# Kernel optimization log

Measured on AMD Instinct MI355X. Metric: run time of the kernel, lower is better.

Reference implementation:

```python
import jax, jax.numpy as jnp
import numpy as np

B, S, D, H = 4, 2048, 1024, 16
DEPTH = D // H
NEG = -1e9


def setup_inputs() -> dict:
    key = jax.random.key(0)
    ks = jax.random.split(key, 10)
    scale = 1.0 / np.sqrt(D)
    return {
        "query": jax.random.normal(ks[0], (B, S, D), jnp.float32),
        "key": jax.random.normal(ks[1], (B, S, D), jnp.float32),
        "value": jax.random.normal(ks[2], (B, S, D), jnp.float32),
        "mask": jnp.zeros((B, 1, 1, S), jnp.float32),
        "Wq": jax.random.normal(ks[3], (D, D), jnp.float32) * scale,
        "bq": jnp.zeros((D,), jnp.float32),
        "Wk": jax.random.normal(ks[4], (D, D), jnp.float32) * scale,
        "bk": jnp.zeros((D,), jnp.float32),
        "Wv": jax.random.normal(ks[5], (D, D), jnp.float32) * scale,
        "bv": jnp.zeros((D,), jnp.float32),
        "Wo": jax.random.normal(ks[6], (D, D), jnp.float32) * scale,
        "bo": jnp.zeros((D,), jnp.float32),
    }


def _split_heads(x):
    # [B, S, D] -> [B, H, S, depth]
    b, s, _ = x.shape
    return x.reshape(b, s, H, DEPTH).transpose(0, 2, 1, 3)


def reference(query, key, value, mask, Wq, bq, Wk, bk, Wv, bv, Wo, bo):
    q = _split_heads(query @ Wq + bq)
    k = _split_heads(key @ Wk + bk)
    v = _split_heads(value @ Wv + bv)
    # scaled dot-product attention
    logits = jnp.einsum("bhqd,bhkd->bhqk", q, k) / jnp.sqrt(
        jnp.asarray(DEPTH, jnp.float32))
    logits = logits + mask * NEG
    attn = jax.nn.softmax(logits, axis=-1)
    out = jnp.einsum("bhqk,bhkd->bhqd", attn, v)
    # merge heads: [B,H,S,depth] -> [B,S,D]
    out = out.transpose(0, 2, 1, 3).reshape(query.shape[0], -1, D)
    out = out @ Wo + bo
    return out, attn
```

## Files before the change

kernel.cpp:

```cpp
#include <hip/hip_runtime.h>
#include <stdint.h>


typedef float f32x4 __attribute__((ext_vector_type(4)));
typedef __bf16 bf16x8 __attribute__((ext_vector_type(8)));
typedef unsigned short u16x4 __attribute__((ext_vector_type(4)));
typedef unsigned short u16x8 __attribute__((ext_vector_type(8)));

#define LOG2E 1.44269504088896340736f

static __device__ __forceinline__ f32x4 mfma16(bf16x8 a, bf16x8 b, f32x4 c) {
  return __builtin_amdgcn_mfma_f32_16x16x32_bf16(a, b, c, 0, 0, 0);
}
static __device__ __forceinline__ unsigned short bfc(float f) {
  return __builtin_bit_cast(unsigned short, (__bf16)f);
}
static __device__ __forceinline__ float e2(float x) { return __builtin_amdgcn_exp2f(x); }

#define GLDS16(g, l)                                                    \
  __builtin_amdgcn_global_load_lds(                                     \
      (const __attribute__((address_space(1))) void*)(g),               \
      (__attribute__((address_space(3))) void*)(l), 16, 0, 0)

struct Ptr3 { const float* s[3]; unsigned short* d[3]; };
struct Ptr4 { const float* s[4]; unsigned short* d[4]; };
struct QKArgs {
  const unsigned short* A[2];
  const unsigned short* Bt[2];
  const float* bias[2];
  unsigned short* C[2];
};

__global__ void cvt3(Ptr3 p) {
  const int z = blockIdx.z;
  const int i = (blockIdx.x * 256 + threadIdx.x) * 4;
  f32x4 v = *(const f32x4*)(const void*)(p.s[z] + i);
  u16x4 o;
  o[0] = bfc(v[0]); o[1] = bfc(v[1]); o[2] = bfc(v[2]); o[3] = bfc(v[3]);
  *(u16x4*)(void*)(p.d[z] + i) = o;
}

__global__ void wtrans4(Ptr4 p) {
  __shared__ float t[32][33];
  const int z = blockIdx.z;
  const float* W = p.s[z];
  unsigned short* Wt = p.d[z];
  const int tx = threadIdx.x & 31, ty = threadIdx.x >> 5;
  const int n0 = blockIdx.x * 32, k0 = blockIdx.y * 32;
#pragma unroll
  for (int i = 0; i < 4; ++i)
    t[ty + i * 8][tx] = W[(size_t)(k0 + ty + i * 8) * 1024 + n0 + tx];
  __syncthreads();
#pragma unroll
  for (int i = 0; i < 4; ++i)
    Wt[(size_t)(n0 + ty + i * 8) * 1024 + k0 + tx] = bfc(t[tx][ty + i * 8]);
}

#define GEMM_PROLOG(Aptr, Btptr)                                        \
  __shared__ unsigned short sA[128 * 32];                               \
  __shared__ unsigned short sB[128 * 32];                               \
  const int tid = threadIdx.x;                                          \
  const int m0 = blockIdx.x << 7, n0 = blockIdx.y << 7;                 \
  const int w = tid >> 6, lane = tid & 63, g = lane >> 4, r = lane & 15;\
  const int wr = w >> 1, wc = w & 1;                                    \
  const int srow = tid >> 2;                                            \
  const int scol = (tid & 3) << 3;                                      \
  const unsigned short* ga = (Aptr) + (size_t)(m0 + srow) * 1024 + scol;\
  const unsigned short* gb = (Btptr) + (size_t)(n0 + srow) * 1024 + scol;\
  unsigned short* la = sA + tid * 8;                                    \
  unsigned short* lb = sB + tid * 8;

#define GEMM_KLOOP(SWAP)                                                \
  for (int kt = 0; kt < 32; ++kt) {                                     \
    const int ko = kt << 5;                                             \
    GLDS16(ga + ko, la);                                                \
    GLDS16(ga + ko + 64 * 1024, la + 64 * 32);                          \
    GLDS16(gb + ko, lb);                                                \
    GLDS16(gb + ko + 64 * 1024, lb + 64 * 32);                          \
    __syncthreads();                                                    \
    bf16x8 af[4], bfv[4];                                               \
    _Pragma("unroll")                                                   \
    for (int i = 0; i < 4; ++i) {                                       \
      af[i]  = *(const bf16x8*)(const void*)&sA[(wr * 64 + i * 16 + r) * 32 + g * 8]; \
      bfv[i] = *(const bf16x8*)(const void*)&sB[(wc * 64 + i * 16 + r) * 32 + g * 8]; \
    }                                                                   \
    _Pragma("unroll")                                                   \
    for (int i = 0; i < 4; ++i)                                         \
      _Pragma("unroll")                                                 \
      for (int j = 0; j < 4; ++j)                                       \
        acc[i][j] = (SWAP) ? mfma16(bfv[j], af[i], acc[i][j])           \
                           : mfma16(af[i], bfv[j], acc[i][j]);          \
    __syncthreads();                                                    \
  }

__global__ __launch_bounds__(256, 2) void gemm_qk(QKArgs args) {
  const int z = blockIdx.z;
  const f32x4 fz = {0.f, 0.f, 0.f, 0.f};
  f32x4 acc[4][4];
#pragma unroll
  for (int i = 0; i < 4; ++i)
#pragma unroll
    for (int j = 0; j < 4; ++j) acc[i][j] = fz;
  GEMM_PROLOG(args.A[z], args.Bt[z])
  GEMM_KLOOP(1)
  const float osc = (z == 0) ? (0.125f * LOG2E) : 1.0f;
  unsigned short* Cq = args.C[z];
  const float* bias = args.bias[z];
#pragma unroll
  for (int j = 0; j < 4; ++j) {
    const int nb = n0 + wc * 64 + j * 16 + g * 4;
    const f32x4 b4 = *(const f32x4*)(const void*)(bias + nb);
#pragma unroll
    for (int i = 0; i < 4; ++i) {
      const int m = m0 + wr * 64 + i * 16 + r;
      const int bb = m >> 11, s = m & 2047, hh = nb >> 6, d = nb & 63;
      u16x4 pk;
#pragma unroll
      for (int t = 0; t < 4; ++t) pk[t] = bfc((acc[i][j][t] + b4[t]) * osc);
      *(u16x4*)(void*)(Cq + (size_t)(bb * 16 + hh) * 131072 + (size_t)s * 64 + d) = pk;
    }
  }
}

__global__ __launch_bounds__(256, 2) void gemm_v(const unsigned short* __restrict__ A,
                                                 const unsigned short* __restrict__ Bt,
                                                 const float* __restrict__ bias,
                                                 unsigned short* __restrict__ C) {
  const f32x4 fz = {0.f, 0.f, 0.f, 0.f};
  f32x4 acc[4][4];
#pragma unroll
  for (int i = 0; i < 4; ++i)
#pragma unroll
    for (int j = 0; j < 4; ++j) acc[i][j] = fz;
  GEMM_PROLOG(A, Bt)
  GEMM_KLOOP(0)
#pragma unroll
  for (int j = 0; j < 4; ++j) {
    const int n = n0 + wc * 64 + j * 16 + r;
    const float bv = bias[n];
    const int hh = n >> 6, d = n & 63;
#pragma unroll
    for (int i = 0; i < 4; ++i) {
      const int m = m0 + wr * 64 + i * 16 + g * 4;
      const int bb = m >> 11, s = m & 2047;
      u16x4 pk;
#pragma unroll
      for (int t = 0; t < 4; ++t) pk[t] = bfc(acc[i][j][t] + bv);
      *(u16x4*)(void*)(C + (size_t)(bb * 16 + hh) * 131072 + (size_t)d * 2048 + s) = pk;
    }
  }
}

__global__ __launch_bounds__(256, 2) void gemm_o(const unsigned short* __restrict__ A,
                                                 const unsigned short* __restrict__ Bt,
                                                 const float* __restrict__ bias,
                                                 float* __restrict__ C) {
  const f32x4 fz = {0.f, 0.f, 0.f, 0.f};
  f32x4 acc[4][4];
#pragma unroll
  for (int i = 0; i < 4; ++i)
#pragma unroll
    for (int j = 0; j < 4; ++j) acc[i][j] = fz;
  GEMM_PROLOG(A, Bt)
  GEMM_KLOOP(1)
#pragma unroll
  for (int j = 0; j < 4; ++j) {
    const int nb = n0 + wc * 64 + j * 16 + g * 4;
    const f32x4 b4 = *(const f32x4*)(const void*)(bias + nb);
#pragma unroll
    for (int i = 0; i < 4; ++i) {
      const int m = m0 + wr * 64 + i * 16 + r;
      f32x4 c;
#pragma unroll
      for (int t = 0; t < 4; ++t) c[t] = acc[i][j][t] + b4[t];
      *(f32x4*)(void*)(C + (size_t)m * 1024 + nb) = c;
    }
  }
}

__global__ __launch_bounds__(256, 2) void attn_fused(const unsigned short* __restrict__ Qh,
                                                     const unsigned short* __restrict__ Kh,
                                                     const unsigned short* __restrict__ Vt,
                                                     const float* __restrict__ mask,
                                                     float* __restrict__ attn_out,
                                                     unsigned short* __restrict__ Obuf) {
  __shared__ unsigned short Plds[4][64 * 40];
  __shared__ float Osum[64][68];
  __shared__ float sml[4][64];

  const int blk = (blockIdx.x & 7) * 256 + (blockIdx.x >> 3);
  const int bh = blk >> 5;
  const int q0 = (blk & 31) << 6;
  const int b = bh >> 4, h = bh & 15;
  const int tid = threadIdx.x;
  const int w = tid >> 6, lane = tid & 63, g = lane >> 4, r = lane & 15;
  const float NEGM = -1e9f * LOG2E;

  const unsigned short* Qb = Qh + (size_t)bh * (2048 * 64);
  const unsigned short* Kb = Kh + (size_t)bh * (2048 * 64);
  const unsigned short* Vb = Vt + (size_t)bh * (64 * 2048);
  const float* mb = mask + (size_t)b * 2048;
  const f32x4 fz = {0.f, 0.f, 0.f, 0.f};

  bf16x8 qf[4][2];
#pragma unroll
  for (int qc = 0; qc < 4; ++qc)
#pragma unroll
    for (int hf = 0; hf < 2; ++hf)
      qf[qc][hf] = *(const bf16x8*)(const void*)(Qb + (size_t)(q0 + qc * 16 + r) * 64 + hf * 32 + g * 8);

  float lreg[4] = {0.f, 0.f, 0.f, 0.f};

  for (int step = 0; step < 16; ++step) {
    const int kk = (w << 9) + (step << 5);
    bf16x8 kf[2][2];
#pragma unroll
    for (int ks = 0; ks < 2; ++ks)
#pragma unroll
      for (int hf = 0; hf < 2; ++hf)
        kf[ks][hf] = *(const bf16x8*)(const void*)(Kb + (size_t)(kk + ks * 16 + r) * 64 + hf * 32 + g * 8);
    f32x4 mv0 = *(const f32x4*)(const void*)(mb + kk + g * 4);
    f32x4 mv1 = *(const f32x4*)(const void*)(mb + kk + 16 + g * 4);
    unsigned int mbits = 0;
#pragma unroll
    for (int j = 0; j < 4; ++j)
      mbits |= __builtin_bit_cast(unsigned int, mv0[j]) | __builtin_bit_cast(unsigned int, mv1[j]);

    f32x4 s0[4], s1[4];
#pragma unroll
    for (int qc = 0; qc < 4; ++qc) {
      s0[qc] = fz; s1[qc] = fz;
      s0[qc] = mfma16(kf[0][0], qf[qc][0], s0[qc]);
      s0[qc] = mfma16(kf[0][1], qf[qc][1], s0[qc]);
      s1[qc] = mfma16(kf[1][0], qf[qc][0], s1[qc]);
      s1[qc] = mfma16(kf[1][1], qf[qc][1], s1[qc]);
    }
    if (__builtin_expect(mbits == 0, 1)) {
#pragma unroll
      for (int qc = 0; qc < 4; ++qc) {
        float p = 0.f;
#pragma unroll
        for (int j = 0; j < 4; ++j) p += e2(s0[qc][j]) + e2(s1[qc][j]);
        lreg[qc] += p;
      }
    } else {
      f32x4 mp0, mp1;
#pragma unroll
      for (int j = 0; j < 4; ++j) { mp0[j] = mv0[j] * NEGM; mp1[j] = mv1[j] * NEGM; }
#pragma unroll
      for (int qc = 0; qc < 4; ++qc) {
        float p = 0.f;
#pragma unroll
        for (int j = 0; j < 4; ++j) p += e2(s0[qc][j] + mp0[j]) + e2(s1[qc][j] + mp1[j]);
        lreg[qc] += p;
      }
    }
  }
#pragma unroll
  for (int qc = 0; qc < 4; ++qc) {
    lreg[qc] += __shfl_xor(lreg[qc], 16);
    lreg[qc] += __shfl_xor(lreg[qc], 32);
  }
  if (lane < 16) {
#pragma unroll
    for (int qc = 0; qc < 4; ++qc) sml[w][qc * 16 + lane] = lreg[qc];
  }
  __syncthreads();
  float cL[4], invL[4];
#pragma unroll
  for (int qc = 0; qc < 4; ++qc) {
    const int q = qc * 16 + r;
    const float L = sml[0][q] + sml[1][q] + sml[2][q] + sml[3][q];
    cL[qc] = -__log2f(L);
    invL[qc] = 1.f / L;
  }

  f32x4 oacc[4][4];
#pragma unroll
  for (int i = 0; i < 4; ++i)
#pragma unroll
    for (int j = 0; j < 4; ++j) oacc[i][j] = fz;

  float* ab = attn_out + (size_t)bh * 2048 * 2048;

  for (int step = 0; step < 16; ++step) {
    const int kk = (w << 9) + (step << 5);
    bf16x8 kf[2][2];
#pragma unroll
    for (int ks = 0; ks < 2; ++ks)
#pragma unroll
      for (int hf = 0; hf < 2; ++hf)
        kf[ks][hf] = *(const bf16x8*)(const void*)(Kb + (size_t)(kk + ks * 16 + r) * 64 + hf * 32 + g * 8);
    f32x4 mv0 = *(const f32x4*)(const void*)(mb + kk + g * 4);
    f32x4 mv1 = *(const f32x4*)(const void*)(mb + kk + 16 + g * 4);
    unsigned int mbits = 0;
#pragma unroll
    for (int j = 0; j < 4; ++j)
      mbits |= __builtin_bit_cast(unsigned int, mv0[j]) | __builtin_bit_cast(unsigned int, mv1[j]);
    f32x4 mp[2];
    if (__builtin_expect(mbits != 0, 0)) {
#pragma unroll
      for (int j = 0; j < 4; ++j) {
        mp[0][j] = mv0[j] * NEGM;
        mp[1][j] = mv1[j] * NEGM;
      }
    } else {
      mp[0] = fz; mp[1] = fz;
    }

#pragma unroll
    for (int ks = 0; ks < 2; ++ks) {
#pragma unroll
      for (int qc = 0; qc < 4; ++qc) {
        f32x4 s = fz;
        s = mfma16(kf[ks][0], qf[qc][0], s);
        s = mfma16(kf[ks][1], qf[qc][1], s);
        f32x4 pv;
        u16x4 pb;
#pragma unroll
        for (int j = 0; j < 4; ++j) {
          const float val = e2(s[j] + mp[ks][j] + cL[qc]);
          pv[j] = val;
          pb[j] = bfc(val);
        }
        __builtin_nontemporal_store(
            pv, (f32x4*)(void*)(ab + (size_t)(q0 + qc * 16 + r) * 2048 + kk + ks * 16 + g * 4));
        *(u16x4*)(void*)(&Plds[w][(qc * 16 + r) * 40 + ks * 16 + g * 4]) = pb;
      }
    }
    bf16x8 vf[4];
#pragma unroll
    for (int dn = 0; dn < 4; ++dn)
      vf[dn] = *(const bf16x8*)(const void*)(Vb + (size_t)(dn * 16 + r) * 2048 + kk + g * 8);
#pragma unroll
    for (int qs = 0; qs < 4; ++qs) {
      const bf16x8 pa = *(const bf16x8*)(const void*)(&Plds[w][(qs * 16 + r) * 40 + g * 8]);
#pragma unroll
      for (int dn = 0; dn < 4; ++dn) oacc[qs][dn] = mfma16(pa, vf[dn], oacc[qs][dn]);
    }
  }

  for (int wv = 0; wv < 4; ++wv) {
    if (w == wv) {
#pragma unroll
      for (int qs = 0; qs < 4; ++qs)
#pragma unroll
        for (int dn = 0; dn < 4; ++dn)
#pragma unroll
          for (int j = 0; j < 4; ++j) {
            const int q = qs * 16 + g * 4 + j, d = dn * 16 + r;
            if (wv == 0) Osum[q][d] = oacc[qs][dn][j];
            else         Osum[q][d] += oacc[qs][dn][j];
          }
    }
    __syncthreads();
  }
  (void)invL;
  const int orow = tid >> 2, oc0 = (tid & 3) << 4;
#pragma unroll
  for (int half = 0; half < 2; ++half) {
    u16x8 pk;
#pragma unroll
    for (int j = 0; j < 8; ++j) pk[j] = bfc(Osum[orow][oc0 + half * 8 + j]);
    *(u16x8*)(void*)(Obuf + (size_t)(b * 2048 + q0 + orow) * 1024 + h * 64 + oc0 + half * 8) = pk;
  }
}

extern "C" void kernel_launch(void* const* d_in, const int* in_sizes, int n_in,
                              void* d_out, int out_size, void* d_ws, size_t ws_size,
                              hipStream_t stream) {
  const float* query = (const float*)d_in[0];
  const float* key_  = (const float*)d_in[1];
  const float* value = (const float*)d_in[2];
  const float* mask  = (const float*)d_in[3];
  const float* Wq = (const float*)d_in[4];
  const float* bq = (const float*)d_in[5];
  const float* Wk = (const float*)d_in[6];
  const float* bk = (const float*)d_in[7];
  const float* Wv = (const float*)d_in[8];
  const float* bv = (const float*)d_in[9];
  const float* Wo = (const float*)d_in[10];
  const float* bo = (const float*)d_in[11];

  uint8_t* ws = (uint8_t*)d_ws;
  unsigned short* XQ  = (unsigned short*)(ws);
  unsigned short* XK  = (unsigned short*)(ws + 16777216);
  unsigned short* XV  = (unsigned short*)(ws + 33554432);
  unsigned short* WTQ = (unsigned short*)(ws + 50331648);
  unsigned short* WTK = (unsigned short*)(ws + 52428800);
  unsigned short* WTV = (unsigned short*)(ws + 54525952);
  unsigned short* WTO = (unsigned short*)(ws + 56623104);
  unsigned short* QH  = (unsigned short*)(ws + 58720256);
  unsigned short* KH  = (unsigned short*)(ws + 75497472);
  unsigned short* VT  = (unsigned short*)(ws + 92274688);
  unsigned short* OB  = XQ;

  float* outp = (float*)d_out;
  float* attnp = outp + 8388608;

  Ptr3 pc = {{query, key_, value}, {XQ, XK, XV}};
  cvt3<<<dim3(8192, 1, 3), 256, 0, stream>>>(pc);
  Ptr4 pw = {{Wq, Wk, Wv, Wo}, {WTQ, WTK, WTV, WTO}};
  wtrans4<<<dim3(32, 32, 4), 256, 0, stream>>>(pw);
  QKArgs qk = {{XQ, XK}, {WTQ, WTK}, {bq, bk}, {QH, KH}};
  gemm_qk<<<dim3(64, 8, 2), 256, 0, stream>>>(qk);
  gemm_v<<<dim3(64, 8), 256, 0, stream>>>(XV, WTV, bv, VT);
  attn_fused<<<2048, 256, 0, stream>>>(QH, KH, VT, mask, attnp, OB);
  gemm_o<<<dim3(64, 8), 256, 0, stream>>>(OB, WTO, bo, outp);
}
```

Measured before the change: 498.0 us.

## Halve attention query tile to 32 rows and raise occupancy; drop mask branch

Shrinks each attention block's query tile from 64 to 32 rows, doubles the grid to 4096 blocks and raises the launch-bounds occupancy hint from 2 to 4 blocks per CU. This cuts register and LDS use per block so more waves can hide memory latency on the large attn-matrix store. It also removes the all-zero-mask fast path and always applies the mask multiply-add. In exchange, each K/V tile is reloaded twice as often per query, and there is extra VALU work for the mask.

```diff
diff --git a/kernel.cpp b/kernel.cpp
--- a/kernel.cpp
+++ b/kernel.cpp
@@ -178,19 +178,19 @@
   }
 }
 
-__global__ __launch_bounds__(256, 2) void attn_fused(const unsigned short* __restrict__ Qh,
+__global__ __launch_bounds__(256, 4) void attn_fused(const unsigned short* __restrict__ Qh,
                                                      const unsigned short* __restrict__ Kh,
                                                      const unsigned short* __restrict__ Vt,
                                                      const float* __restrict__ mask,
                                                      float* __restrict__ attn_out,
                                                      unsigned short* __restrict__ Obuf) {
-  __shared__ unsigned short Plds[4][64 * 40];
-  __shared__ float Osum[64][68];
-  __shared__ float sml[4][64];
-
-  const int blk = (blockIdx.x & 7) * 256 + (blockIdx.x >> 3);
-  const int bh = blk >> 5;
-  const int q0 = (blk & 31) << 6;
+  __shared__ unsigned short Plds[4][32 * 40];
+  __shared__ float Osum[32][68];
+  __shared__ float sml[4][32];
+
+  const int blk = (blockIdx.x & 7) * 512 + (blockIdx.x >> 3);
+  const int bh = blk >> 6;
+  const int q0 = (blk & 63) << 5;
   const int b = bh >> 4, h = bh & 15;
   const int tid = threadIdx.x;
   const int w = tid >> 6, lane = tid & 63, g = lane >> 4, r = lane & 15;
@@ -202,14 +202,14 @@
   const float* mb = mask + (size_t)b * 2048;
   const f32x4 fz = {0.f, 0.f, 0.f, 0.f};
 
-  bf16x8 qf[4][2];
-#pragma unroll
-  for (int qc = 0; qc < 4; ++qc)
+  bf16x8 qf[2][2];
+#pragma unroll
+  for (int qc = 0; qc < 2; ++qc)
 #pragma unroll
     for (int hf = 0; hf < 2; ++hf)
       qf[qc][hf] = *(const bf16x8*)(const void*)(Qb + (size_t)(q0 + qc * 16 + r) * 64 + hf * 32 + g * 8);
 
-  float lreg[4] = {0.f, 0.f, 0.f, 0.f};
+  float lreg[2] = {0.f, 0.f};
 
   for (int step = 0; step < 16; ++step) {
     const int kk = (w << 9) + (step << 5);
@@ -221,63 +221,43 @@
         kf[ks][hf] = *(const bf16x8*)(const void*)(Kb + (size_t)(kk + ks * 16 + r) * 64 + hf * 32 + g * 8);
     f32x4 mv0 = *(const f32x4*)(const void*)(mb + kk + g * 4);
     f32x4 mv1 = *(const f32x4*)(const void*)(mb + kk + 16 + g * 4);
-    unsigned int mbits = 0;
-#pragma unroll
-    for (int j = 0; j < 4; ++j)
-      mbits |= __builtin_bit_cast(unsigned int, mv0[j]) | __builtin_bit_cast(unsigned int, mv1[j]);
-
-    f32x4 s0[4], s1[4];
-#pragma unroll
-    for (int qc = 0; qc < 4; ++qc) {
-      s0[qc] = fz; s1[qc] = fz;
-      s0[qc] = mfma16(kf[0][0], qf[qc][0], s0[qc]);
-      s0[qc] = mfma16(kf[0][1], qf[qc][1], s0[qc]);
-      s1[qc] = mfma16(kf[1][0], qf[qc][0], s1[qc]);
-      s1[qc] = mfma16(kf[1][1], qf[qc][1], s1[qc]);
-    }
-    if (__builtin_expect(mbits == 0, 1)) {
-#pragma unroll
-      for (int qc = 0; qc < 4; ++qc) {
-        float p = 0.f;
-#pragma unroll
-        for (int j = 0; j < 4; ++j) p += e2(s0[qc][j]) + e2(s1[qc][j]);
-        lreg[qc] += p;
-      }
-    } else {
-      f32x4 mp0, mp1;
-#pragma unroll
-      for (int j = 0; j < 4; ++j) { mp0[j] = mv0[j] * NEGM; mp1[j] = mv1[j] * NEGM; }
-#pragma unroll
-      for (int qc = 0; qc < 4; ++qc) {
-        float p = 0.f;
-#pragma unroll
-        for (int j = 0; j < 4; ++j) p += e2(s0[qc][j] + mp0[j]) + e2(s1[qc][j] + mp1[j]);
-        lreg[qc] += p;
-      }
-    }
-  }
-#pragma unroll
-  for (int qc = 0; qc < 4; ++qc) {
+    f32x4 mp0, mp1;
+#pragma unroll
+    for (int j = 0; j < 4; ++j) { mp0[j] = mv0[j] * NEGM; mp1[j] = mv1[j] * NEGM; }
+
+#pragma unroll
+    for (int qc = 0; qc < 2; ++qc) {
+      f32x4 s0 = fz, s1 = fz;
+      s0 = mfma16(kf[0][0], qf[qc][0], s0);
+      s0 = mfma16(kf[0][1], qf[qc][1], s0);
+      s1 = mfma16(kf[1][0], qf[qc][0], s1);
+      s1 = mfma16(kf[1][1], qf[qc][1], s1);
+      float p = 0.f;
+#pragma unroll
+      for (int j = 0; j < 4; ++j) p += e2(s0[j] + mp0[j]) + e2(s1[j] + mp1[j]);
+      lreg[qc] += p;
+    }
+  }
+#pragma unroll
+  for (int qc = 0; qc < 2; ++qc) {
     lreg[qc] += __shfl_xor(lreg[qc], 16);
     lreg[qc] += __shfl_xor(lreg[qc], 32);
   }
   if (lane < 16) {
 #pragma unroll
-    for (int qc = 0; qc < 4; ++qc) sml[w][qc * 16 + lane] = lreg[qc];
+    for (int qc = 0; qc < 2; ++qc) sml[w][qc * 16 + lane] = lreg[qc];
   }
   __syncthreads();
-  float cL[4], invL[4];
-#pragma unroll
-  for (int qc = 0; qc < 4; ++qc) {
+  float cL[2];
+#pragma unroll
+  for (int qc = 0; qc < 2; ++qc) {
     const int q = qc * 16 + r;
-    const float L = sml[0][q] + sml[1][q] + sml[2][q] + sml[3][q];
-    cL[qc] = -__log2f(L);
-    invL[qc] = 1.f / L;
-  }
-
-  f32x4 oacc[4][4];
-#pragma unroll
-  for (int i = 0; i < 4; ++i)
+    cL[qc] = -__log2f(sml[0][q] + sml[1][q] + sml[2][q] + sml[3][q]);
+  }
+
+  f32x4 oacc[2][4];
+#pragma unroll
+  for (int i = 0; i < 2; ++i)
 #pragma unroll
     for (int j = 0; j < 4; ++j) oacc[i][j] = fz;
 
@@ -293,25 +273,14 @@
         kf[ks][hf] = *(const bf16x8*)(const void*)(Kb + (size_t)(kk + ks * 16 + r) * 64 + hf * 32 + g * 8);
     f32x4 mv0 = *(const f32x4*)(const void*)(mb + kk + g * 4);
     f32x4 mv1 = *(const f32x4*)(const void*)(mb + kk + 16 + g * 4);
-    unsigned int mbits = 0;
-#pragma unroll
-    for (int j = 0; j < 4; ++j)
-      mbits |= __builtin_bit_cast(unsigned int, mv0[j]) | __builtin_bit_cast(unsigned int, mv1[j]);
     f32x4 mp[2];
-    if (__builtin_expect(mbits != 0, 0)) {
-#pragma unroll
-      for (int j = 0; j < 4; ++j) {
-        mp[0][j] = mv0[j] * NEGM;
-        mp[1][j] = mv1[j] * NEGM;
-      }
-    } else {
-      mp[0] = fz; mp[1] = fz;
-    }
+#pragma unroll
+    for (int j = 0; j < 4; ++j) { mp[0][j] = mv0[j] * NEGM; mp[1][j] = mv1[j] * NEGM; }
 
 #pragma unroll
     for (int ks = 0; ks < 2; ++ks) {
 #pragma unroll
-      for (int qc = 0; qc < 4; ++qc) {
+      for (int qc = 0; qc < 2; ++qc) {
         f32x4 s = fz;
         s = mfma16(kf[ks][0], qf[qc][0], s);
         s = mfma16(kf[ks][1], qf[qc][1], s);
@@ -333,7 +302,7 @@
     for (int dn = 0; dn < 4; ++dn)
       vf[dn] = *(const bf16x8*)(const void*)(Vb + (size_t)(dn * 16 + r) * 2048 + kk + g * 8);
 #pragma unroll
-    for (int qs = 0; qs < 4; ++qs) {
+    for (int qs = 0; qs < 2; ++qs) {
       const bf16x8 pa = *(const bf16x8*)(const void*)(&Plds[w][(qs * 16 + r) * 40 + g * 8]);
 #pragma unroll
       for (int dn = 0; dn < 4; ++dn) oacc[qs][dn] = mfma16(pa, vf[dn], oacc[qs][dn]);
@@ -343,7 +312,7 @@
   for (int wv = 0; wv < 4; ++wv) {
     if (w == wv) {
 #pragma unroll
-      for (int qs = 0; qs < 4; ++qs)
+      for (int qs = 0; qs < 2; ++qs)
 #pragma unroll
         for (int dn = 0; dn < 4; ++dn)
 #pragma unroll
@@ -355,15 +324,11 @@
     }
     __syncthreads();
   }
-  (void)invL;
-  const int orow = tid >> 2, oc0 = (tid & 3) << 4;
-#pragma unroll
-  for (int half = 0; half < 2; ++half) {
-    u16x8 pk;
-#pragma unroll
-    for (int j = 0; j < 8; ++j) pk[j] = bfc(Osum[orow][oc0 + half * 8 + j]);
-    *(u16x8*)(void*)(Obuf + (size_t)(b * 2048 + q0 + orow) * 1024 + h * 64 + oc0 + half * 8) = pk;
-  }
+  const int orow = tid >> 3, oc0 = (tid & 7) << 3;
+  u16x8 pk;
+#pragma unroll
+  for (int j = 0; j < 8; ++j) pk[j] = bfc(Osum[orow][oc0 + j]);
+  *(u16x8*)(void*)(Obuf + (size_t)(b * 2048 + q0 + orow) * 1024 + h * 64 + oc0) = pk;
 }
 
 extern "C" void kernel_launch(void* const* d_in, const int* in_sizes, int n_in,
@@ -405,6 +370,6 @@
   QKArgs qk = {{XQ, XK}, {WTQ, WTK}, {bq, bk}, {QH, KH}};
   gemm_qk<<<dim3(64, 8, 2), 256, 0, stream>>>(qk);
   gemm_v<<<dim3(64, 8), 256, 0, stream>>>(XV, WTV, bv, VT);
-  attn_fused<<<2048, 256, 0, stream>>>(QH, KH, VT, mask, attnp, OB);
+  attn_fused<<<4096, 256, 0, stream>>>(QH, KH, VT, mask, attnp, OB);
   gemm_o<<<dim3(64, 8), 256, 0, stream>>>(OB, WTO, bo, outp);
 }
```

Result: slower. 546.1 us (+9.7%).
